# Kernel optimization log

Measured on AMD Instinct MI355X. Metric: run time of the kernel, lower is better.

The kernel has to match this reference:

```python
import jax, jax.numpy as jnp
import numpy as np

NEG_INF = -1e9  # Keras uses a large negative for masked logits


def setup_inputs() -> dict:
    key = jax.random.key(0)
    k1, k2, k3, k4, k5 = jax.random.split(key, 5)
    B, Tq, Tv, D, U = 8, 128, 128, 512, 1024
    query = jax.random.normal(k1, (B, Tq, D), dtype=jnp.float32)
    value = jax.random.normal(k2, (B, Tv, D), dtype=jnp.float32)
    mask = jnp.ones((B, Tv), dtype=bool)
    # Dense(units, use_bias=False) kernels and AdditiveAttention scale vector
    W1 = jax.random.normal(k3, (D, U), dtype=jnp.float32) * (1.0 / np.sqrt(D))
    W2 = jax.random.normal(k4, (D, U), dtype=jnp.float32) * (1.0 / np.sqrt(D))
    scale = jax.random.normal(k5, (U,), dtype=jnp.float32) * (1.0 / np.sqrt(U))
    return {"query": query, "value": value, "mask": mask,
            "W1": W1, "W2": W2, "scale": scale}


def reference(query, value, mask, W1, W2, scale):
    # Projections (Dense, no bias)
    wq = jnp.einsum('btd,du->btu', query, W1)   # [B, Tq, U]
    wk = jnp.einsum('bsd,du->bsu', value, W2)   # [B, Tv, U]
    # Additive (Bahdanau) scores: sum_u scale_u * tanh(wq + wk)
    # Materializes [B, Tq, Tv, U] broadcast-add like Keras AdditiveAttention.
    scores = jnp.einsum('u,btsu->bts', scale,
                        jnp.tanh(wq[:, :, None, :] + wk[:, None, :, :]))
    # value mask over key axis (query_mask is all-ones in the source -> no-op)
    scores = jnp.where(mask[:, None, :], scores, NEG_INF)
    attn = jax.nn.softmax(scores, axis=-1)       # [B, Tq, Tv]
    context = jnp.einsum('bts,bsd->btd', attn, value)  # [B, Tq, D]
    return context, attn
```

## Files before the change

### kernel.cpp

```cpp
#include <hip/hip_runtime.h>

#define B_  8
#define TQ  128
#define TV  128
#define DIM 512
#define UU  1024
#define NSPLIT 16
#define NP  (B_ * TQ * TV)
#define C2  2.885390081777927f

typedef __attribute__((ext_vector_type(8))) short     short8;
typedef __attribute__((ext_vector_type(4))) float     f32x4;
typedef __attribute__((ext_vector_type(4))) unsigned short us4;

__device__ __forceinline__ unsigned short bf16_rtne(float x) {
    unsigned u = __float_as_uint(x);
    unsigned r = u + 0x7FFF + ((u >> 16) & 1);
    return (unsigned short)(r >> 16);
}
__device__ __forceinline__ float bf16_to_f(unsigned short h) {
    return __uint_as_float(((unsigned)h) << 16);
}

__global__ __launch_bounds__(256) void k_prep(
    const float* __restrict__ Q, const float* __restrict__ Vv,
    const float* __restrict__ W1, const float* __restrict__ W2,
    unsigned short* __restrict__ Ah, unsigned short* __restrict__ Al,
    unsigned short* __restrict__ Wh, unsigned short* __restrict__ Wl)
{
    __shared__ float ts[32][36];
    const int bx = blockIdx.x;
    const int t  = threadIdx.x;

    if (bx < 1024) {
        int idx = bx * 256 + t;
        int mat = idx >> 17;
        const float* src = mat ? Vv : Q;
        int off = (idx & 131071) * 4;
        float4 v = *(const float4*)&src[off];
        us4 h, l;
        h.x = bf16_rtne(v.x); l.x = bf16_rtne(v.x - bf16_to_f(h.x));
        h.y = bf16_rtne(v.y); l.y = bf16_rtne(v.y - bf16_to_f(h.y));
        h.z = bf16_rtne(v.z); l.z = bf16_rtne(v.z - bf16_to_f(h.z));
        h.w = bf16_rtne(v.w); l.w = bf16_rtne(v.w - bf16_to_f(h.w));
        *(us4*)&Ah[mat * 524288 + off] = h;
        *(us4*)&Al[mat * 524288 + off] = l;
    } else {
        int b2   = bx - 1024;
        int mat  = b2 >> 9;
        int tile = b2 & 511;
        int n0 = (tile & 31) * 32;
        int k0 = (tile >> 5) * 32;
        const float* W = mat ? W2 : W1;

        int kk = t >> 3, n4 = (t & 7) * 4;
        float4 w = *(const float4*)&W[(k0 + kk) * UU + n0 + n4];
        ts[n4 + 0][kk] = w.x; ts[n4 + 1][kk] = w.y;
        ts[n4 + 2][kk] = w.z; ts[n4 + 3][kk] = w.w;
        __syncthreads();

        int nn = t >> 3, k4 = (t & 7) * 4;
        float4 v = *(const float4*)&ts[nn][k4];
        us4 h, l;
        h.x = bf16_rtne(v.x); l.x = bf16_rtne(v.x - bf16_to_f(h.x));
        h.y = bf16_rtne(v.y); l.y = bf16_rtne(v.y - bf16_to_f(h.y));
        h.z = bf16_rtne(v.z); l.z = bf16_rtne(v.z - bf16_to_f(h.z));
        h.w = bf16_rtne(v.w); l.w = bf16_rtne(v.w - bf16_to_f(h.w));
        unsigned off = mat * 524288 + (n0 + nn) * 512 + k0 + k4;
        *(us4*)&Wh[off] = h;
        *(us4*)&Wl[off] = l;
    }
}

#define PKP 72
__global__ __launch_bounds__(256) void k_proj(
    const unsigned short* __restrict__ Ah, const unsigned short* __restrict__ Al,
    const unsigned short* __restrict__ Bh, const unsigned short* __restrict__ Bl,
    float* __restrict__ Eq, float* __restrict__ Ek)
{
    __shared__ short sAh[64 * PKP], sAl[64 * PKP], sBh[64 * PKP], sBl[64 * PKP];

    const int tid  = threadIdx.x;
    const int wave = tid >> 6;
    const int lane = tid & 63;

    const int flat = blockIdx.x;
    const int x    = flat & 7;
    const int j    = flat >> 3;
    const int pair = x * 4 + (j >> 4);
    const int nt   = pair & 15;
    const int mat  = pair >> 4;
    const int mt   = j & 15;
    const int m0   = mt * 64;
    const int n0   = nt * 64;

    const unsigned mb = mat * 524288u;
    const int wm = (wave & 1) * 32;
    const int wn = (wave >> 1) * 32;

    const int sm = tid >> 2, sg = tid & 3;
    const unsigned short* gAh = Ah + mb + (m0 + sm) * 512;
    const unsigned short* gAl = Al + mb + (m0 + sm) * 512;
    const unsigned short* gBh = Bh + mb + (n0 + sm) * 512;
    const unsigned short* gBl = Bl + mb + (n0 + sm) * 512;
    const int so0 = sm * PKP + sg * 8;
    const int so1 = sm * PKP + 32 + sg * 8;

    const int fr = lane & 15, fq = lane >> 4;
    const int aOff0 = (wm + fr) * PKP + fq * 8;
    const int aOff1 = (wm + 16 + fr) * PKP + fq * 8;
    const int bOff0 = (wn + fr) * PKP + fq * 8;
    const int bOff1 = (wn + 16 + fr) * PKP + fq * 8;

    f32x4 acc00 = {0.f, 0.f, 0.f, 0.f};
    f32x4 acc01 = {0.f, 0.f, 0.f, 0.f};
    f32x4 acc10 = {0.f, 0.f, 0.f, 0.f};
    f32x4 acc11 = {0.f, 0.f, 0.f, 0.f};

    int4 rAh0, rAh1, rAl0, rAl1, rBh0, rBh1, rBl0, rBl1;
    #define LOADALL(K)                                                       \
        rAh0 = *(const int4*)(gAh + (K) + sg * 8);                           \
        rAh1 = *(const int4*)(gAh + (K) + 32 + sg * 8);                      \
        rAl0 = *(const int4*)(gAl + (K) + sg * 8);                           \
        rAl1 = *(const int4*)(gAl + (K) + 32 + sg * 8);                      \
        rBh0 = *(const int4*)(gBh + (K) + sg * 8);                           \
        rBh1 = *(const int4*)(gBh + (K) + 32 + sg * 8);                      \
        rBl0 = *(const int4*)(gBl + (K) + sg * 8);                           \
        rBl1 = *(const int4*)(gBl + (K) + 32 + sg * 8);

    LOADALL(0)

    #pragma unroll 1
    for (int kc = 0; kc < 8; ++kc) {
        *(int4*)&sAh[so0] = rAh0;  *(int4*)&sAh[so1] = rAh1;
        *(int4*)&sAl[so0] = rAl0;  *(int4*)&sAl[so1] = rAl1;
        *(int4*)&sBh[so0] = rBh0;  *(int4*)&sBh[so1] = rBh1;
        *(int4*)&sBl[so0] = rBl0;  *(int4*)&sBl[so1] = rBl1;
        __syncthreads();

        if (kc < 7) { LOADALL((kc + 1) * 64) }

        #pragma unroll
        for (int ks = 0; ks < 2; ++ks) {
            const int o = ks * 32;
            short8 a0h = *(const short8*)&sAh[aOff0 + o];
            short8 a0l = *(const short8*)&sAl[aOff0 + o];
            short8 a1h = *(const short8*)&sAh[aOff1 + o];
            short8 a1l = *(const short8*)&sAl[aOff1 + o];
            short8 b0h = *(const short8*)&sBh[bOff0 + o];
            short8 b0l = *(const short8*)&sBl[bOff0 + o];
            short8 b1h = *(const short8*)&sBh[bOff1 + o];
            short8 b1l = *(const short8*)&sBl[bOff1 + o];

            acc00 = __builtin_amdgcn_mfma_f32_16x16x32_bf16(a0h, b0h, acc00, 0, 0, 0);
            acc00 = __builtin_amdgcn_mfma_f32_16x16x32_bf16(a0h, b0l, acc00, 0, 0, 0);
            acc00 = __builtin_amdgcn_mfma_f32_16x16x32_bf16(a0l, b0h, acc00, 0, 0, 0);

            acc01 = __builtin_amdgcn_mfma_f32_16x16x32_bf16(a0h, b1h, acc01, 0, 0, 0);
            acc01 = __builtin_amdgcn_mfma_f32_16x16x32_bf16(a0h, b1l, acc01, 0, 0, 0);
            acc01 = __builtin_amdgcn_mfma_f32_16x16x32_bf16(a0l, b1h, acc01, 0, 0, 0);

            acc10 = __builtin_amdgcn_mfma_f32_16x16x32_bf16(a1h, b0h, acc10, 0, 0, 0);
            acc10 = __builtin_amdgcn_mfma_f32_16x16x32_bf16(a1h, b0l, acc10, 0, 0, 0);
            acc10 = __builtin_amdgcn_mfma_f32_16x16x32_bf16(a1l, b0h, acc10, 0, 0, 0);

            acc11 = __builtin_amdgcn_mfma_f32_16x16x32_bf16(a1h, b1h, acc11, 0, 0, 0);
            acc11 = __builtin_amdgcn_mfma_f32_16x16x32_bf16(a1h, b1l, acc11, 0, 0, 0);
            acc11 = __builtin_amdgcn_mfma_f32_16x16x32_bf16(a1l, b1h, acc11, 0, 0, 0);
        }
        __syncthreads();
    }
    #undef LOADALL

    float* C = mat ? Ek : Eq;
    #pragma unroll
    for (int r = 0; r < 4; ++r) {
        int row0 = m0 + wm + fq * 4 + r;
        int row1 = row0 + 16;
        int col0 = n0 + wn + fr;
        C[row0 * UU + col0]      = __builtin_amdgcn_exp2f(C2 * acc00[r]);
        C[row0 * UU + col0 + 16] = __builtin_amdgcn_exp2f(C2 * acc01[r]);
        C[row1 * UU + col0]      = __builtin_amdgcn_exp2f(C2 * acc10[r]);
        C[row1 * UU + col0 + 16] = __builtin_amdgcn_exp2f(C2 * acc11[r]);
    }
}
#undef PKP

__global__ __launch_bounds__(256) void k_scores(
    const float* __restrict__ Eq, const float* __restrict__ Ek,
    const float* __restrict__ scale, float* __restrict__ part)
{
    __shared__ float qs[64][68];
    __shared__ float ks[64][68];
    __shared__ float ss[64];

    const int tid = threadIdx.x;
    const int tx  = tid & 15;
    const int ty  = tid >> 4;
    const int b   = blockIdx.z & 7;
    const int us  = blockIdx.z >> 3;
    const int t0  = blockIdx.y * 64;
    const int s0  = blockIdx.x * 64;
    const int u0  = us * (UU / NSPLIT);

    {
        const int r  = tid >> 2;
        const int c0 = (tid & 3) * 16;
        const float* srq = &Eq[(b * TQ + t0 + r) * UU + u0 + c0];
        const float* srk = &Ek[(b * TV + s0 + r) * UU + u0 + c0];
        const int rp = (r >> 2) | ((r & 3) << 4);
        #pragma unroll
        for (int i = 0; i < 4; ++i) {
            *(float4*)&qs[r][c0 + i * 4]  = *(const float4*)(srq + i * 4);
            *(float4*)&ks[rp][c0 + i * 4] = *(const float4*)(srk + i * 4);
        }
        if (tid < 16)
            *(float4*)&ss[tid * 4] = *(const float4*)&scale[u0 + tid * 4];
    }
    __syncthreads();

    float acc[4][4] = {};

    #pragma unroll 2
    for (int u4 = 0; u4 < 16; ++u4) {
        float4 q[4], k[4];
        #pragma unroll
        for (int i = 0; i < 4; ++i)
            q[i] = *(const float4*)&qs[ty * 4 + i][u4 * 4];
        #pragma unroll
        for (int jj = 0; jj < 4; ++jj)
            k[jj] = *(const float4*)&ks[tx + (jj << 4)][u4 * 4];
        float4 sv = *(const float4*)&ss[u4 * 4];

        #pragma unroll
        for (int i = 0; i < 4; ++i) {
            #pragma unroll
            for (int jj = 0; jj < 4; ++jj) {
                float p1 = q[i].x * k[jj].x, p2 = q[i].y * k[jj].y;
                float b1 = p1 + 1.f,        b2 = p2 + 1.f;
                float n1 = fmaf(sv.y, b1, sv.x * b2);
                acc[i][jj] = fmaf(n1, __builtin_amdgcn_rcpf(b1 * b2), acc[i][jj]);
                float p3 = q[i].z * k[jj].z, p4 = q[i].w * k[jj].w;
                float b3 = p3 + 1.f,        b4 = p4 + 1.f;
                float n2 = fmaf(sv.w, b3, sv.z * b4);
                acc[i][jj] = fmaf(n2, __builtin_amdgcn_rcpf(b3 * b4), acc[i][jj]);
            }
        }
    }

    #pragma unroll
    for (int i = 0; i < 4; ++i) {
        float4 o = {acc[i][0], acc[i][1], acc[i][2], acc[i][3]};
        *(float4*)&part[us * NP + (b * TQ + t0 + ty * 4 + i) * TV + s0 + tx * 4] = o;
    }
}

__global__ __launch_bounds__(256) void k_ctx(
    const float* __restrict__ part, const int* __restrict__ mask,
    const float* __restrict__ Vv,
    float* __restrict__ attn, float* __restrict__ ctx)
{
    __shared__ float at[128][20];

    const int tid = threadIdx.x;
    const int dc  = blockIdx.x;
    const int tt  = blockIdx.y;
    const int b   = blockIdx.z;
    const int t0  = tt * 16;
    const int rg  = tid >> 4;
    const int ln  = tid & 15;
    const int base = (b * TQ + t0 + rg) * TV;

    float x[8];
    #pragma unroll
    for (int j = 0; j < 8; ++j) {
        const int s = ln + 16 * j;
        float p = 0.f;
        #pragma unroll
        for (int i = 0; i < NSPLIT; ++i) p += part[i * NP + base + s];
        x[j] = mask[b * TV + s] ? -2.f * p : -1e9f;
    }
    float m = x[0];
    #pragma unroll
    for (int j = 1; j < 8; ++j) m = fmaxf(m, x[j]);
    #pragma unroll
    for (int o = 8; o > 0; o >>= 1) m = fmaxf(m, __shfl_xor(m, o, 64));
    const float L2E = 1.4426950408889634f;
    float e[8];
    float sum = 0.f;
    #pragma unroll
    for (int j = 0; j < 8; ++j) {
        e[j] = __builtin_amdgcn_exp2f((x[j] - m) * L2E);
        sum += e[j];
    }
    #pragma unroll
    for (int o = 8; o > 0; o >>= 1) sum += __shfl_xor(sum, o, 64);
    const float r = __builtin_amdgcn_rcpf(sum);
    #pragma unroll
    for (int j = 0; j < 8; ++j) {
        const float a = e[j] * r;
        at[ln + 16 * j][rg] = a;
        if (dc == 0) attn[base + ln + 16 * j] = a;
    }
    __syncthreads();

    const int d  = (tid & 127) + dc * 128;
    const int tg = tid >> 7;
    float acc[8] = {};
    const float* vp = &Vv[b * TV * DIM + d];
    for (int s = 0; s < TV; ++s) {
        float v = vp[s * DIM];
        float4 a0 = *(const float4*)&at[s][tg * 8];
        float4 a1 = *(const float4*)&at[s][tg * 8 + 4];
        acc[0] = fmaf(a0.x, v, acc[0]);
        acc[1] = fmaf(a0.y, v, acc[1]);
        acc[2] = fmaf(a0.z, v, acc[2]);
        acc[3] = fmaf(a0.w, v, acc[3]);
        acc[4] = fmaf(a1.x, v, acc[4]);
        acc[5] = fmaf(a1.y, v, acc[5]);
        acc[6] = fmaf(a1.z, v, acc[6]);
        acc[7] = fmaf(a1.w, v, acc[7]);
    }
    #pragma unroll
    for (int j = 0; j < 8; ++j) {
        int t = t0 + tg * 8 + j;
        ctx[(b * TQ + t) * DIM + d] = acc[j];
    }
}

extern "C" void kernel_launch(void* const* d_in, const int* in_sizes, int n_in,
                              void* d_out, int out_size, void* d_ws, size_t ws_size,
                              hipStream_t stream)
{
    const float* query = (const float*)d_in[0];
    const float* value = (const float*)d_in[1];
    const int*   mask  = (const int*)d_in[2];
    const float* W1    = (const float*)d_in[3];
    const float* W2    = (const float*)d_in[4];
    const float* scale = (const float*)d_in[5];

    float* out  = (float*)d_out;
    float* ctx  = out;
    float* attn = out + B_ * TQ * DIM;

    float* Eq   = (float*)d_ws;
    float* Ek   = Eq + 1024 * 1024;
    float* part = Ek + 1024 * 1024;
    unsigned short* Ah = (unsigned short*)(part + NSPLIT * NP);
    unsigned short* Al = Ah + 2 * 1024 * 512;
    unsigned short* Wh = Al + 2 * 1024 * 512;
    unsigned short* Wl = Wh + 2 * 1024 * 512;

    hipLaunchKernelGGL(k_prep,   dim3(2048),             dim3(256), 0, stream,
                       query, value, W1, W2, Ah, Al, Wh, Wl);
    hipLaunchKernelGGL(k_proj,   dim3(512),              dim3(256), 0, stream,
                       Ah, Al, Wh, Wl, Eq, Ek);
    hipLaunchKernelGGL(k_scores, dim3(2, 2, 8 * NSPLIT), dim3(256), 0, stream,
                       Eq, Ek, scale, part);
    hipLaunchKernelGGL(k_ctx,    dim3(4, 8, 8),          dim3(256), 0, stream,
                       part, mask, value, attn, ctx);
}
```

Baseline: 113.7 us.

## Drop low-bf16 weight term in projection and halve query rows per ctx block

The split-bf16 projection GEMM drops the weight low-part term: W is now stored as a single bf16 while the activations keep their hi+lo split. This removes a third of the MFMAs, one LDS buffer and the Wl global traffic, at the cost of reduced accuracy in the projections. Separately, the context kernel now handles 8 query rows per block instead of 16, doubling the grid to raise parallelism. That change adds redundant reads of the score partials and V.

```diff
diff --git a/kernel.cpp b/kernel.cpp
--- a/kernel.cpp
+++ b/kernel.cpp
@@ -26,7 +26,7 @@
     const float* __restrict__ Q, const float* __restrict__ Vv,
     const float* __restrict__ W1, const float* __restrict__ W2,
     unsigned short* __restrict__ Ah, unsigned short* __restrict__ Al,
-    unsigned short* __restrict__ Wh, unsigned short* __restrict__ Wl)
+    unsigned short* __restrict__ Wh)
 {
     __shared__ float ts[32][36];
     const int bx = blockIdx.x;
@@ -61,24 +61,23 @@
 
         int nn = t >> 3, k4 = (t & 7) * 4;
         float4 v = *(const float4*)&ts[nn][k4];
-        us4 h, l;
-        h.x = bf16_rtne(v.x); l.x = bf16_rtne(v.x - bf16_to_f(h.x));
-        h.y = bf16_rtne(v.y); l.y = bf16_rtne(v.y - bf16_to_f(h.y));
-        h.z = bf16_rtne(v.z); l.z = bf16_rtne(v.z - bf16_to_f(h.z));
-        h.w = bf16_rtne(v.w); l.w = bf16_rtne(v.w - bf16_to_f(h.w));
+        us4 h;
+        h.x = bf16_rtne(v.x);
+        h.y = bf16_rtne(v.y);
+        h.z = bf16_rtne(v.z);
+        h.w = bf16_rtne(v.w);
         unsigned off = mat * 524288 + (n0 + nn) * 512 + k0 + k4;
         *(us4*)&Wh[off] = h;
-        *(us4*)&Wl[off] = l;
     }
 }
 
 #define PKP 72
 __global__ __launch_bounds__(256) void k_proj(
     const unsigned short* __restrict__ Ah, const unsigned short* __restrict__ Al,
-    const unsigned short* __restrict__ Bh, const unsigned short* __restrict__ Bl,
+    const unsigned short* __restrict__ Bh,
     float* __restrict__ Eq, float* __restrict__ Ek)
 {
-    __shared__ short sAh[64 * PKP], sAl[64 * PKP], sBh[64 * PKP], sBl[64 * PKP];
+    __shared__ short sAh[64 * PKP], sAl[64 * PKP], sBh[64 * PKP];
 
     const int tid  = threadIdx.x;
     const int wave = tid >> 6;
@@ -102,7 +101,6 @@
     const unsigned short* gAh = Ah + mb + (m0 + sm) * 512;
     const unsigned short* gAl = Al + mb + (m0 + sm) * 512;
     const unsigned short* gBh = Bh + mb + (n0 + sm) * 512;
-    const unsigned short* gBl = Bl + mb + (n0 + sm) * 512;
     const int so0 = sm * PKP + sg * 8;
     const int so1 = sm * PKP + 32 + sg * 8;
 
@@ -117,16 +115,14 @@
     f32x4 acc10 = {0.f, 0.f, 0.f, 0.f};
     f32x4 acc11 = {0.f, 0.f, 0.f, 0.f};
 
-    int4 rAh0, rAh1, rAl0, rAl1, rBh0, rBh1, rBl0, rBl1;
+    int4 rAh0, rAh1, rAl0, rAl1, rBh0, rBh1;
     #define LOADALL(K)                                                       \
         rAh0 = *(const int4*)(gAh + (K) + sg * 8);                           \
         rAh1 = *(const int4*)(gAh + (K) + 32 + sg * 8);                      \
         rAl0 = *(const int4*)(gAl + (K) + sg * 8);                           \
         rAl1 = *(const int4*)(gAl + (K) + 32 + sg * 8);                      \
         rBh0 = *(const int4*)(gBh + (K) + sg * 8);                           \
-        rBh1 = *(const int4*)(gBh + (K) + 32 + sg * 8);                      \
-        rBl0 = *(const int4*)(gBl + (K) + sg * 8);                           \
-        rBl1 = *(const int4*)(gBl + (K) + 32 + sg * 8);
+        rBh1 = *(const int4*)(gBh + (K) + 32 + sg * 8);
 
     LOADALL(0)
 
@@ -135,7 +131,6 @@
         *(int4*)&sAh[so0] = rAh0;  *(int4*)&sAh[so1] = rAh1;
         *(int4*)&sAl[so0] = rAl0;  *(int4*)&sAl[so1] = rAl1;
         *(int4*)&sBh[so0] = rBh0;  *(int4*)&sBh[so1] = rBh1;
-        *(int4*)&sBl[so0] = rBl0;  *(int4*)&sBl[so1] = rBl1;
         __syncthreads();
 
         if (kc < 7) { LOADALL((kc + 1) * 64) }
@@ -148,24 +143,18 @@
             short8 a1h = *(const short8*)&sAh[aOff1 + o];
             short8 a1l = *(const short8*)&sAl[aOff1 + o];
             short8 b0h = *(const short8*)&sBh[bOff0 + o];
-            short8 b0l = *(const short8*)&sBl[bOff0 + o];
             short8 b1h = *(const short8*)&sBh[bOff1 + o];
-            short8 b1l = *(const short8*)&sBl[bOff1 + o];
 
             acc00 = __builtin_amdgcn_mfma_f32_16x16x32_bf16(a0h, b0h, acc00, 0, 0, 0);
-            acc00 = __builtin_amdgcn_mfma_f32_16x16x32_bf16(a0h, b0l, acc00, 0, 0, 0);
             acc00 = __builtin_amdgcn_mfma_f32_16x16x32_bf16(a0l, b0h, acc00, 0, 0, 0);
 
             acc01 = __builtin_amdgcn_mfma_f32_16x16x32_bf16(a0h, b1h, acc01, 0, 0, 0);
-            acc01 = __builtin_amdgcn_mfma_f32_16x16x32_bf16(a0h, b1l, acc01, 0, 0, 0);
             acc01 = __builtin_amdgcn_mfma_f32_16x16x32_bf16(a0l, b1h, acc01, 0, 0, 0);
 
             acc10 = __builtin_amdgcn_mfma_f32_16x16x32_bf16(a1h, b0h, acc10, 0, 0, 0);
-            acc10 = __builtin_amdgcn_mfma_f32_16x16x32_bf16(a1h, b0l, acc10, 0, 0, 0);
             acc10 = __builtin_amdgcn_mfma_f32_16x16x32_bf16(a1l, b0h, acc10, 0, 0, 0);
 
             acc11 = __builtin_amdgcn_mfma_f32_16x16x32_bf16(a1h, b1h, acc11, 0, 0, 0);
-            acc11 = __builtin_amdgcn_mfma_f32_16x16x32_bf16(a1h, b1l, acc11, 0, 0, 0);
             acc11 = __builtin_amdgcn_mfma_f32_16x16x32_bf16(a1l, b1h, acc11, 0, 0, 0);
         }
         __syncthreads();
@@ -260,70 +249,63 @@
     const float* __restrict__ Vv,
     float* __restrict__ attn, float* __restrict__ ctx)
 {
-    __shared__ float at[128][20];
+    __shared__ float at[128][12];
 
     const int tid = threadIdx.x;
     const int dc  = blockIdx.x;
     const int tt  = blockIdx.y;
     const int b   = blockIdx.z;
-    const int t0  = tt * 16;
-    const int rg  = tid >> 4;
-    const int ln  = tid & 15;
+    const int t0  = tt * 8;
+    const int rg  = tid >> 5;
+    const int ln  = tid & 31;
     const int base = (b * TQ + t0 + rg) * TV;
 
-    float x[8];
-    #pragma unroll
-    for (int j = 0; j < 8; ++j) {
-        const int s = ln + 16 * j;
+    float x[4];
+    #pragma unroll
+    for (int j = 0; j < 4; ++j) {
+        const int s = ln + 32 * j;
         float p = 0.f;
         #pragma unroll
         for (int i = 0; i < NSPLIT; ++i) p += part[i * NP + base + s];
         x[j] = mask[b * TV + s] ? -2.f * p : -1e9f;
     }
-    float m = x[0];
-    #pragma unroll
-    for (int j = 1; j < 8; ++j) m = fmaxf(m, x[j]);
-    #pragma unroll
-    for (int o = 8; o > 0; o >>= 1) m = fmaxf(m, __shfl_xor(m, o, 64));
+    float m = fmaxf(fmaxf(x[0], x[1]), fmaxf(x[2], x[3]));
+    #pragma unroll
+    for (int o = 16; o > 0; o >>= 1) m = fmaxf(m, __shfl_xor(m, o, 64));
     const float L2E = 1.4426950408889634f;
-    float e[8];
-    float sum = 0.f;
-    #pragma unroll
-    for (int j = 0; j < 8; ++j) {
+    float e[4], sum = 0.f;
+    #pragma unroll
+    for (int j = 0; j < 4; ++j) {
         e[j] = __builtin_amdgcn_exp2f((x[j] - m) * L2E);
         sum += e[j];
     }
     #pragma unroll
-    for (int o = 8; o > 0; o >>= 1) sum += __shfl_xor(sum, o, 64);
+    for (int o = 16; o > 0; o >>= 1) sum += __shfl_xor(sum, o, 64);
     const float r = __builtin_amdgcn_rcpf(sum);
     #pragma unroll
-    for (int j = 0; j < 8; ++j) {
+    for (int j = 0; j < 4; ++j) {
         const float a = e[j] * r;
-        at[ln + 16 * j][rg] = a;
-        if (dc == 0) attn[base + ln + 16 * j] = a;
+        at[ln + 32 * j][rg] = a;
+        if (dc == 0) attn[base + ln + 32 * j] = a;
     }
     __syncthreads();
 
     const int d  = (tid & 127) + dc * 128;
     const int tg = tid >> 7;
-    float acc[8] = {};
+    float acc[4] = {};
     const float* vp = &Vv[b * TV * DIM + d];
+    #pragma unroll 4
     for (int s = 0; s < TV; ++s) {
-        float v = vp[s * DIM];
-        float4 a0 = *(const float4*)&at[s][tg * 8];
-        float4 a1 = *(const float4*)&at[s][tg * 8 + 4];
-        acc[0] = fmaf(a0.x, v, acc[0]);
-        acc[1] = fmaf(a0.y, v, acc[1]);
-        acc[2] = fmaf(a0.z, v, acc[2]);
-        acc[3] = fmaf(a0.w, v, acc[3]);
-        acc[4] = fmaf(a1.x, v, acc[4]);
-        acc[5] = fmaf(a1.y, v, acc[5]);
-        acc[6] = fmaf(a1.z, v, acc[6]);
-        acc[7] = fmaf(a1.w, v, acc[7]);
-    }
-    #pragma unroll
-    for (int j = 0; j < 8; ++j) {
-        int t = t0 + tg * 8 + j;
+        float v  = vp[s * DIM];
+        float4 a = *(const float4*)&at[s][tg * 4];
+        acc[0] = fmaf(a.x, v, acc[0]);
+        acc[1] = fmaf(a.y, v, acc[1]);
+        acc[2] = fmaf(a.z, v, acc[2]);
+        acc[3] = fmaf(a.w, v, acc[3]);
+    }
+    #pragma unroll
+    for (int j = 0; j < 4; ++j) {
+        int t = t0 + tg * 4 + j;
         ctx[(b * TQ + t) * DIM + d] = acc[j];
     }
 }
@@ -349,14 +331,13 @@
     unsigned short* Ah = (unsigned short*)(part + NSPLIT * NP);
     unsigned short* Al = Ah + 2 * 1024 * 512;
     unsigned short* Wh = Al + 2 * 1024 * 512;
-    unsigned short* Wl = Wh + 2 * 1024 * 512;
 
     hipLaunchKernelGGL(k_prep,   dim3(2048),             dim3(256), 0, stream,
-                       query, value, W1, W2, Ah, Al, Wh, Wl);
+                       query, value, W1, W2, Ah, Al, Wh);
     hipLaunchKernelGGL(k_proj,   dim3(512),              dim3(256), 0, stream,
-                       Ah, Al, Wh, Wl, Eq, Ek);
+                       Ah, Al, Wh, Eq, Ek);
     hipLaunchKernelGGL(k_scores, dim3(2, 2, 8 * NSPLIT), dim3(256), 0, stream,
                        Eq, Ek, scale, part);
-    hipLaunchKernelGGL(k_ctx,    dim3(4, 8, 8),          dim3(256), 0, stream,
+    hipLaunchKernelGGL(k_ctx,    dim3(4, 16, 8),         dim3(256), 0, stream,
                        part, mask, value, attn, ctx);
 }
```

Result: no change. 112.8 us (-0.8%).
